# Kernel optimization log

Hardware: AMD Instinct MI355X
Metric: run time of the kernel (lower is better)

The kernel has to match this reference:

```python
import jax, jax.numpy as jnp
import numpy as np

NEG_SLOPE = 0.2  # PyG GATConv default negative_slope


def gat_conv(x, src, dst, num_nodes, W, att_src, att_dst, bias, heads, out_ch, concat):
    """PyG-style GATConv (eval mode, self-loops already included in src/dst).
    x: [N, in]; W: [in, heads*out_ch]; att_*: [heads, out_ch]; bias: [heads*out_ch] or [out_ch].
    """
    N = num_nodes
    h = (x @ W).reshape(N, heads, out_ch)                      # [N, H, C]
    a_src = jnp.sum(h * att_src[None], axis=-1)                 # [N, H]
    a_dst = jnp.sum(h * att_dst[None], axis=-1)                 # [N, H]
    e = a_src[src] + a_dst[dst]                                 # [E, H]
    e = jnp.where(e > 0, e, NEG_SLOPE * e)                      # leaky_relu
    # segment softmax over incoming edges of each destination node
    m = jax.ops.segment_max(e, dst, num_segments=N)             # [N, H]
    w = jnp.exp(e - m[dst])                                     # [E, H]
    denom = jax.ops.segment_sum(w, dst, num_segments=N)         # [N, H]
    alpha = w / denom[dst]                                      # [E, H]
    out = jax.ops.segment_sum(h[src] * alpha[:, :, None], dst, num_segments=N)  # [N, H, C]
    if concat:
        out = out.reshape(N, heads * out_ch)
    else:
        out = out.mean(axis=1)
    return out + bias


def setup_inputs() -> dict:
    key = jax.random.key(0)
    ks = jax.random.split(key, 20)
    N, T, F_IN = 100000, 50, 10
    E = 1600000
    H1, C1 = 4, 32          # conv1: heads=4, hidden=32 -> 128
    LAT = 64                # latent_dim

    def g(k, shape, scale):
        return (jax.random.normal(k, shape, dtype=jnp.float32) * scale)

    inp = {
        "temporal_data": jax.random.normal(ks[0], (N, T, F_IN), dtype=jnp.float32),
        "x": jax.random.normal(ks[1], (N, F_IN), dtype=jnp.float32),
        "edge_index": jax.random.randint(ks[2], (2, E), 0, N, dtype=jnp.int32),
        # temporal encoder: Linear(10,64) -> ReLU -> Linear(64,64)
        "tW1": g(ks[3], (F_IN, 64), 0.3), "tb1": jnp.zeros((64,), jnp.float32),
        "tW2": g(ks[4], (64, LAT), 0.12), "tb2": jnp.zeros((LAT,), jnp.float32),
        # GATConv1: in=10, out=32, heads=4, concat
        "gW1": g(ks[5], (F_IN, H1 * C1), 0.3),
        "ga1_src": g(ks[6], (H1, C1), 0.17), "ga1_dst": g(ks[7], (H1, C1), 0.17),
        "gb1": jnp.zeros((H1 * C1,), jnp.float32),
        # GATConv2: in=128, out=64, heads=1, concat=False
        "gW2": g(ks[8], (H1 * C1, LAT), 0.09),
        "ga2_src": g(ks[9], (1, LAT), 0.12), "ga2_dst": g(ks[10], (1, LAT), 0.12),
        "gb2": jnp.zeros((LAT,), jnp.float32),
        # classifier: Linear(128,64) -> ReLU -> (Dropout eval) -> Linear(64,1) -> Sigmoid
        "cW1": g(ks[11], (2 * LAT, 64), 0.09), "cb1": jnp.zeros((64,), jnp.float32),
        "cW2": g(ks[12], (64, 1), 0.12), "cb2": jnp.zeros((1,), jnp.float32),
    }
    return inp


def reference(temporal_data, x, edge_index, tW1, tb1, tW2, tb2,
              gW1, ga1_src, ga1_dst, gb1, gW2, ga2_src, ga2_dst, gb2,
              cW1, cb1, cW2, cb2):
    N = x.shape[0]
    # temporal encoder then mean over time axis (dim=1)
    t = jax.nn.relu(temporal_data @ tW1 + tb1) @ tW2 + tb2      # [N, T, 64]
    t = t.mean(axis=1)                                           # [N, 64]
    # add self-loops (PyG GATConv default add_self_loops=True)
    loop = jnp.arange(N, dtype=edge_index.dtype)
    src = jnp.concatenate([edge_index[0], loop])
    dst = jnp.concatenate([edge_index[1], loop])
    h = gat_conv(x, src, dst, N, gW1, ga1_src, ga1_dst, gb1, heads=4, out_ch=32, concat=True)
    h = jax.nn.elu(h)
    g = gat_conv(h, src, dst, N, gW2, ga2_src, ga2_dst, gb2, heads=1, out_ch=64, concat=False)  # [N, 64]
    combined = jnp.concatenate([t, g], axis=-1)                  # [N, 128]
    z = jax.nn.relu(combined @ cW1 + cb1) @ cW2 + cb2            # [N, 1]
    return jax.nn.sigmoid(z)
```

## Files before the change

kernel.cpp:

```cpp
#include <hip/hip_runtime.h>
#include <hip/hip_bf16.h>

#define DEV_INLINE __device__ __forceinline__

typedef __attribute__((ext_vector_type(8))) short short8v;
typedef __attribute__((ext_vector_type(4))) float f32x4;

DEV_INLINE float lrelu(float v) { return fmaxf(v, 0.2f * v); }

DEV_INLINE unsigned int cvt_pk_bf16(float lo, float hi) {
    unsigned int r;
    asm("v_cvt_pk_bf16_f32 %0, %1, %2" : "=v"(r) : "v"(lo), "v"(hi));
    return r;
}

DEV_INLINE unsigned short f2bf_rne(float f) {
    unsigned int b = __float_as_uint(f);
    return (unsigned short)((b + 0x7FFFu + ((b >> 16) & 1u)) >> 16);
}

DEV_INLINE unsigned int pack_bf16(float lo, float hi) {
    return (unsigned int)f2bf_rne(lo) | ((unsigned int)f2bf_rne(hi) << 16);
}

DEV_INLINE float bf_lo(unsigned int u) { return __uint_as_float(u << 16); }
DEV_INLINE float bf_hi(unsigned int u) { return __uint_as_float(u & 0xFFFF0000u); }

__global__ __launch_bounds__(1024) void k_scan1(const int* __restrict__ counts,
                                                int* __restrict__ rowptr,
                                                int* __restrict__ partials, int N) {
    __shared__ int sd[1024];
    int li = threadIdx.x;
    int i  = blockIdx.x * 1024 + li;
    int v  = (i < N) ? counts[i] : 0;
    sd[li] = v;
    __syncthreads();
    for (int off = 1; off < 1024; off <<= 1) {
        int t = (li >= off) ? sd[li - off] : 0;
        __syncthreads();
        sd[li] += t;
        __syncthreads();
    }
    int inc = sd[li];
    if (i < N) rowptr[i + 1] = inc;
    if (li == 1023) partials[blockIdx.x] = inc;
}

__global__ void k_scan3(int* __restrict__ rowptr, const int* __restrict__ partials,
                        int* __restrict__ nxt, int N) {
    int i = blockIdx.x * blockDim.x + threadIdx.x;
    if (i > N) return;
    int v;
    if (i == 0) { v = 0; rowptr[0] = 0; }
    else {
        int blk = (i - 1) >> 10;
        int pp = 0;
        for (int b = 0; b < blk; ++b) pp += partials[b];
        v = rowptr[i] + pp;
        rowptr[i] = v;
    }
    if (i < N) nxt[i] = v;
}

#define SC_K 8
#define SC_P 16
__global__ __launch_bounds__(256) void k_scatter(const int* __restrict__ ei,
                                                 int* __restrict__ nxt,
                                                 int* __restrict__ col,
                                                 int E, int range) {
    int t = threadIdx.x;
    int base = blockIdx.x * (256 * SC_K);
    int s[SC_K], d[SC_K];
#pragma unroll
    for (int k = 0; k < SC_K; ++k) {
        int e = base + k * 256 + t;
        bool v = (e < E);
        s[k] = v ? ei[e] : 0;
        d[k] = v ? ei[E + e] : -1;
    }
    int lo = 0;
    for (int p = 0; p < SC_P; ++p, lo += range) {
        int hi = lo + range;
#pragma unroll
        for (int k = 0; k < SC_K; ++k) {
            if (d[k] >= lo && d[k] < hi) {
                int pos = atomicAdd(&nxt[d[k]], 1);
                col[pos] = s[k];
            }
        }
        __syncthreads();
    }
}

__global__ __launch_bounds__(256) void k_temporal(const float* __restrict__ td,
                                                  const float* __restrict__ tW1,
                                                  const float* __restrict__ tb1,
                                                  const int* __restrict__ ei,
                                                  int* __restrict__ counts,
                                                  const float* __restrict__ tW2,
                                                  const float* __restrict__ cW1,
                                                  const float* __restrict__ tb2,
                                                  const float* __restrict__ cb1,
                                                  unsigned short* __restrict__ Wf,
                                                  float* __restrict__ bcf,
                                                  unsigned short* __restrict__ mb,
                                                  int N, int E) {
    __shared__ float lds[4][2][512];
    int tid = threadIdx.x, lane = tid & 63, wv = tid >> 6;
    int gid = blockIdx.x * 256 + tid;

    int estr = gridDim.x * 256;
    for (int e = gid; e < E; e += estr) atomicAdd(&counts[ei[E + e]], 1);

    if (gid < 4096) {
        int i = gid >> 6, c = gid & 63;
        float s = 0.f;
#pragma unroll 8
        for (int k = 0; k < 64; ++k) s = fmaf(tW2[i * 64 + k], cW1[k * 64 + c], s);
        Wf[gid] = f2bf_rne(s);
    } else if (gid < 8192) {
        Wf[gid] = f2bf_rne(cW1[gid]);
    } else if (gid < 8256) {
        int c = gid - 8192;
        float s = cb1[c];
#pragma unroll 8
        for (int k = 0; k < 64; ++k) s = fmaf(tb2[k], cW1[k * 64 + c], s);
        bcf[c] = s;
    }

    int wid  = blockIdx.x * 4 + wv;
    int nwav = gridDim.x * 4;
    int col  = lane & 15;
    int g    = lane >> 4;

    int chunk = (N + nwav - 1) / nwav;
    int n0 = wid * chunk;
    int n1 = min(n0 + chunk, N);
    if (n0 >= n1) return;
    int cnt = n1 - n0;

    short8v B[4];
#pragma unroll
    for (int cb = 0; cb < 4; ++cb) {
        union { short8v v; unsigned short u[8]; } bu;
#pragma unroll
        for (int j = 0; j < 8; ++j) {
            int f = g * 8 + j;
            int c = cb * 16 + col;
            float w = (f < 10) ? tW1[f * 64 + c] : ((f == 10) ? tb1[c] : 0.f);
            bu.u[j] = f2bf_rne(w);
        }
        B[cb] = bu.v;
    }

    float* buf0 = lds[wv][0];
    float* buf1 = lds[wv][1];

    {
        const float4* r4 = reinterpret_cast<const float4*>(td + (size_t)n0 * 500);
        float4 va = r4[lane];
        float4 vb = (lane < 61) ? r4[64 + lane] : make_float4(0.f, 0.f, 0.f, 0.f);
        *reinterpret_cast<float4*>(buf0 + 4 * lane) = va;
        if (lane < 61) *reinterpret_cast<float4*>(buf0 + 256 + 4 * lane) = vb;
    }
    float4 va = make_float4(0.f, 0.f, 0.f, 0.f), vb = va;
    if (cnt > 1) {
        const float4* rn = reinterpret_cast<const float4*>(td + (size_t)(n0 + 1) * 500);
        va = rn[lane];
        if (lane < 61) vb = rn[64 + lane];
    }

    for (int i = 0; i < cnt; ++i) {
        int n = n0 + i;
        float* wb  = (i & 1) ? buf1 : buf0;
        float* wbn = (i & 1) ? buf0 : buf1;

        if (i + 1 < cnt) {
            *reinterpret_cast<float4*>(wbn + 4 * lane) = va;
            if (lane < 61) *reinterpret_cast<float4*>(wbn + 256 + 4 * lane) = vb;
        }
        if (i + 2 < cnt) {
            const float4* rn = reinterpret_cast<const float4*>(td + (size_t)(n + 2) * 500);
            va = rn[lane];
            if (lane < 61) vb = rn[64 + lane];
        }

        float sum0 = 0.f, sum1 = 0.f, sum2 = 0.f, sum3 = 0.f;
#pragma unroll
        for (int tt = 0; tt < 4; ++tt) {
            int t = tt * 16 + col;
            bool valid = (t < 50);
            float x0 = 0.f, x1 = 0.f, x2 = 0.f, x3 = 0.f;
            float x4 = 0.f, x5 = 0.f, x6 = 0.f, x7 = 0.f;
            const float* rp = wb + t * 10;
            if (g == 0 && valid) {
                float2 p0 = *reinterpret_cast<const float2*>(rp);
                float2 p1 = *reinterpret_cast<const float2*>(rp + 2);
                float2 p2 = *reinterpret_cast<const float2*>(rp + 4);
                float2 p3 = *reinterpret_cast<const float2*>(rp + 6);
                x0 = p0.x; x1 = p0.y; x2 = p1.x; x3 = p1.y;
                x4 = p2.x; x5 = p2.y; x6 = p3.x; x7 = p3.y;
            } else if (g == 1 && valid) {
                float2 p4 = *reinterpret_cast<const float2*>(rp + 8);
                x0 = p4.x; x1 = p4.y; x2 = 1.0f;
            }
            union { short8v v; unsigned int w[4]; } au;
            au.w[0] = cvt_pk_bf16(x0, x1);
            au.w[1] = cvt_pk_bf16(x2, x3);
            au.w[2] = cvt_pk_bf16(x4, x5);
            au.w[3] = cvt_pk_bf16(x6, x7);

            f32x4 z = {0.f, 0.f, 0.f, 0.f};
            f32x4 c0 = __builtin_amdgcn_mfma_f32_16x16x32_bf16(au.v, B[0], z, 0, 0, 0);
            f32x4 c1 = __builtin_amdgcn_mfma_f32_16x16x32_bf16(au.v, B[1], z, 0, 0, 0);
            f32x4 c2 = __builtin_amdgcn_mfma_f32_16x16x32_bf16(au.v, B[2], z, 0, 0, 0);
            f32x4 c3 = __builtin_amdgcn_mfma_f32_16x16x32_bf16(au.v, B[3], z, 0, 0, 0);
#pragma unroll
            for (int i2 = 0; i2 < 4; ++i2) {
                sum0 += fmaxf(c0[i2], 0.f);
                sum1 += fmaxf(c1[i2], 0.f);
                sum2 += fmaxf(c2[i2], 0.f);
                sum3 += fmaxf(c3[i2], 0.f);
            }
        }
        sum0 += __shfl_xor(sum0, 16); sum0 += __shfl_xor(sum0, 32);
        sum1 += __shfl_xor(sum1, 16); sum1 += __shfl_xor(sum1, 32);
        sum2 += __shfl_xor(sum2, 16); sum2 += __shfl_xor(sum2, 32);
        sum3 += __shfl_xor(sum3, 16); sum3 += __shfl_xor(sum3, 32);
        float mv = (g == 0) ? sum0 : (g == 1) ? sum1 : (g == 2) ? sum2 : sum3;
        mb[(size_t)n * 64 + lane] = f2bf_rne(mv * 0.02f);
    }
}

__global__ __launch_bounds__(256) void k_g1a(const float* __restrict__ x,
                                             const float* __restrict__ gW1,
                                             const float* __restrict__ as_w,
                                             const float* __restrict__ ad_w,
                                             unsigned short* __restrict__ h1b,
                                             float* __restrict__ a1s,
                                             float* __restrict__ a1d, int N) {
    int tid = threadIdx.x, lane = tid & 63;
    int n0 = blockIdx.x * 4 + (tid >> 6);
    int n  = __builtin_amdgcn_readfirstlane(n0 < N ? n0 : N - 1);

    float wa[10], wb[10];
#pragma unroll
    for (int i = 0; i < 10; ++i) { wa[i] = gW1[i * 128 + lane]; wb[i] = gW1[i * 128 + 64 + lane]; }
    const float* xp = x + (size_t)n * 10;
    float ha = 0.f, hb = 0.f;
#pragma unroll
    for (int i = 0; i < 10; ++i) { float xv = xp[i]; ha = fmaf(xv, wa[i], ha); hb = fmaf(xv, wb[i], hb); }

    int c = lane & 31;
    int headA = lane >> 5;
    float ps_a = ha * as_w[headA * 32 + c];
    float ps_b = hb * as_w[(headA + 2) * 32 + c];
    float pd_a = ha * ad_w[headA * 32 + c];
    float pd_b = hb * ad_w[(headA + 2) * 32 + c];
#pragma unroll
    for (int m = 1; m < 32; m <<= 1) {
        ps_a += __shfl_xor(ps_a, m); ps_b += __shfl_xor(ps_b, m);
        pd_a += __shfl_xor(pd_a, m); pd_b += __shfl_xor(pd_b, m);
    }
    if (n0 < N) {
        h1b[(size_t)n * 128 + lane]      = f2bf_rne(ha);
        h1b[(size_t)n * 128 + 64 + lane] = f2bf_rne(hb);
        if (c == 0) {
            a1s[n * 4 + headA]     = ps_a;
            a1s[n * 4 + 2 + headA] = ps_b;
            a1d[n * 4 + headA]     = pd_a;
            a1d[n * 4 + 2 + headA] = pd_b;
        }
    }
}

__global__ __launch_bounds__(256) void k_g1b(const int* __restrict__ rowptr,
                                             const int* __restrict__ col,
                                             const unsigned int* __restrict__ h1u,
                                             const float* __restrict__ a1s,
                                             const float* __restrict__ a1d,
                                             const float* __restrict__ gb1,
                                             unsigned int* __restrict__ out1u, int N) {
    int tid = threadIdx.x, lane = tid & 63;
    int n0 = blockIdx.x * 4 + (tid >> 6);
    int n  = __builtin_amdgcn_readfirstlane(n0 < N ? n0 : N - 1);

    int start = rowptr[n], end = rowptr[n + 1];
    int q = lane >> 4, c = lane & 15;
    int hsel = c >> 2;
    float advh = a1d[n * 4 + hsel];
    const uint4* h1q = reinterpret_cast<const uint4*>(h1u);

    float den = 0.f;
    float a0 = 0.f, a1v = 0.f, a2v = 0.f, a3v = 0.f;
    float a4 = 0.f, a5 = 0.f, a6 = 0.f, a7 = 0.f;
    if (q == 0) {
        float w = __expf(lrelu(a1s[n * 4 + hsel] + advh));
        uint4 u = h1q[(size_t)n * 16 + c];
        den = w;
        a0 = w * bf_lo(u.x); a1v = w * bf_hi(u.x);
        a2v = w * bf_lo(u.y); a3v = w * bf_hi(u.y);
        a4 = w * bf_lo(u.z); a5 = w * bf_hi(u.z);
        a6 = w * bf_lo(u.w); a7 = w * bf_hi(u.w);
    }
    int e = start + q;
    for (; e + 4 < end; e += 8) {
        int s0 = col[e], s1 = col[e + 4];
        float q0 = a1s[s0 * 4 + hsel];
        float q1 = a1s[s1 * 4 + hsel];
        uint4 u0 = h1q[(size_t)s0 * 16 + c];
        uint4 u1 = h1q[(size_t)s1 * 16 + c];
        float w0 = __expf(lrelu(q0 + advh));
        float w1 = __expf(lrelu(q1 + advh));
        den += w0 + w1;
        a0 = fmaf(w0, bf_lo(u0.x), a0); a1v = fmaf(w0, bf_hi(u0.x), a1v);
        a2v = fmaf(w0, bf_lo(u0.y), a2v); a3v = fmaf(w0, bf_hi(u0.y), a3v);
        a4 = fmaf(w0, bf_lo(u0.z), a4); a5 = fmaf(w0, bf_hi(u0.z), a5);
        a6 = fmaf(w0, bf_lo(u0.w), a6); a7 = fmaf(w0, bf_hi(u0.w), a7);
        a0 = fmaf(w1, bf_lo(u1.x), a0); a1v = fmaf(w1, bf_hi(u1.x), a1v);
        a2v = fmaf(w1, bf_lo(u1.y), a2v); a3v = fmaf(w1, bf_hi(u1.y), a3v);
        a4 = fmaf(w1, bf_lo(u1.z), a4); a5 = fmaf(w1, bf_hi(u1.z), a5);
        a6 = fmaf(w1, bf_lo(u1.w), a6); a7 = fmaf(w1, bf_hi(u1.w), a7);
    }
    if (e < end) {
        int s = col[e];
        float qv = a1s[s * 4 + hsel];
        uint4 u = h1q[(size_t)s * 16 + c];
        float w = __expf(lrelu(qv + advh));
        den += w;
        a0 = fmaf(w, bf_lo(u.x), a0); a1v = fmaf(w, bf_hi(u.x), a1v);
        a2v = fmaf(w, bf_lo(u.y), a2v); a3v = fmaf(w, bf_hi(u.y), a3v);
        a4 = fmaf(w, bf_lo(u.z), a4); a5 = fmaf(w, bf_hi(u.z), a5);
        a6 = fmaf(w, bf_lo(u.w), a6); a7 = fmaf(w, bf_hi(u.w), a7);
    }
#define RED2(v) v += __shfl_xor(v, 16); v += __shfl_xor(v, 32);
    RED2(den) RED2(a0) RED2(a1v) RED2(a2v) RED2(a3v)
    RED2(a4) RED2(a5) RED2(a6) RED2(a7)
#undef RED2

    if (n0 < N && lane < 16) {
        float inv = 1.f / den;
        float v0 = a0 * inv + gb1[8 * c + 0];
        float v1 = a1v * inv + gb1[8 * c + 1];
        float v2 = a2v * inv + gb1[8 * c + 2];
        float v3 = a3v * inv + gb1[8 * c + 3];
        float v4 = a4 * inv + gb1[8 * c + 4];
        float v5 = a5 * inv + gb1[8 * c + 5];
        float v6 = a6 * inv + gb1[8 * c + 6];
        float v7 = a7 * inv + gb1[8 * c + 7];
        v0 = (v0 > 0.f) ? v0 : (__expf(v0) - 1.f);
        v1 = (v1 > 0.f) ? v1 : (__expf(v1) - 1.f);
        v2 = (v2 > 0.f) ? v2 : (__expf(v2) - 1.f);
        v3 = (v3 > 0.f) ? v3 : (__expf(v3) - 1.f);
        v4 = (v4 > 0.f) ? v4 : (__expf(v4) - 1.f);
        v5 = (v5 > 0.f) ? v5 : (__expf(v5) - 1.f);
        v6 = (v6 > 0.f) ? v6 : (__expf(v6) - 1.f);
        v7 = (v7 > 0.f) ? v7 : (__expf(v7) - 1.f);
        uint4 o;
        o.x = pack_bf16(v0, v1); o.y = pack_bf16(v2, v3);
        o.z = pack_bf16(v4, v5); o.w = pack_bf16(v6, v7);
        *reinterpret_cast<uint4*>(out1u + (size_t)n * 64 + 4 * c) = o;
    }
}

__global__ __launch_bounds__(256) void k_g2a(const unsigned short* __restrict__ out1b,
                                             const float* __restrict__ gW2,
                                             const float* __restrict__ a2sw,
                                             const float* __restrict__ a2dw,
                                             unsigned short* __restrict__ h2b,
                                             float* __restrict__ a2s,
                                             float* __restrict__ a2d, int N) {
    int lane = threadIdx.x & 63;
    int wid  = (blockIdx.x * blockDim.x + threadIdx.x) >> 6;
    int nwav = (gridDim.x * blockDim.x) >> 6;
    int col = lane & 15, g4 = lane >> 4;

    short8v Bf[4][4];
#pragma unroll
    for (int ks = 0; ks < 4; ++ks)
#pragma unroll
        for (int cb = 0; cb < 4; ++cb) {
            union { short8v v; unsigned short u[8]; } bu;
#pragma unroll
            for (int j = 0; j < 8; ++j)
                bu.u[j] = f2bf_rne(gW2[(ks * 32 + g4 * 8 + j) * 64 + cb * 16 + col]);
            Bf[ks][cb] = bu.v;
        }
    float asv[4], adv[4];
#pragma unroll
    for (int cb = 0; cb < 4; ++cb) { asv[cb] = a2sw[cb * 16 + col]; adv[cb] = a2dw[cb * 16 + col]; }

    int ntile = (N + 15) >> 4;
    for (int t = wid; t < ntile; t += nwav) {
        int n0 = t * 16;
        int node = n0 + col; if (node >= N) node = N - 1;
        const unsigned short* xr = out1b + (size_t)node * 128;
        f32x4 acc0 = {0.f, 0.f, 0.f, 0.f}, acc1 = acc0, acc2 = acc0, acc3 = acc0;
#pragma unroll
        for (int ks = 0; ks < 4; ++ks) {
            short8v a = *reinterpret_cast<const short8v*>(xr + ks * 32 + g4 * 8);
            acc0 = __builtin_amdgcn_mfma_f32_16x16x32_bf16(a, Bf[ks][0], acc0, 0, 0, 0);
            acc1 = __builtin_amdgcn_mfma_f32_16x16x32_bf16(a, Bf[ks][1], acc1, 0, 0, 0);
            acc2 = __builtin_amdgcn_mfma_f32_16x16x32_bf16(a, Bf[ks][2], acc2, 0, 0, 0);
            acc3 = __builtin_amdgcn_mfma_f32_16x16x32_bf16(a, Bf[ks][3], acc3, 0, 0, 0);
        }
        float ps[4] = {0.f, 0.f, 0.f, 0.f}, pd[4] = {0.f, 0.f, 0.f, 0.f};
#define G2A_EPI(CB, ACC)                                                      \
        {                                                                     \
            _Pragma("unroll")                                                 \
            for (int i = 0; i < 4; ++i) {                                     \
                float v = ACC[i];                                             \
                int r = n0 + g4 * 4 + i;                                      \
                if (r < N) h2b[(size_t)r * 64 + CB * 16 + col] = f2bf_rne(v); \
                ps[i] = fmaf(v, asv[CB], ps[i]);                              \
                pd[i] = fmaf(v, adv[CB], pd[i]);                              \
            }                                                                 \
        }
        G2A_EPI(0, acc0) G2A_EPI(1, acc1) G2A_EPI(2, acc2) G2A_EPI(3, acc3)
#undef G2A_EPI
#pragma unroll
        for (int i = 0; i < 4; ++i) {
            ps[i] += __shfl_xor(ps[i], 1); ps[i] += __shfl_xor(ps[i], 2);
            ps[i] += __shfl_xor(ps[i], 4); ps[i] += __shfl_xor(ps[i], 8);
            pd[i] += __shfl_xor(pd[i], 1); pd[i] += __shfl_xor(pd[i], 2);
            pd[i] += __shfl_xor(pd[i], 4); pd[i] += __shfl_xor(pd[i], 8);
        }
        if (col == 0) {
#pragma unroll
            for (int i = 0; i < 4; ++i) {
                int r = n0 + g4 * 4 + i;
                if (r < N) { a2s[r] = ps[i]; a2d[r] = pd[i]; }
            }
        }
    }
}

__global__ __launch_bounds__(256) void k_g2b(const int* __restrict__ rowptr,
                                             const int* __restrict__ col,
                                             const unsigned int* __restrict__ h2u,
                                             const float* __restrict__ a2s,
                                             const float* __restrict__ a2d,
                                             const float* __restrict__ gb2,
                                             unsigned int* __restrict__ gu, int N) {
    int tid = threadIdx.x, lane = tid & 63;
    int n0 = blockIdx.x * 4 + (tid >> 6);
    int n  = __builtin_amdgcn_readfirstlane(n0 < N ? n0 : N - 1);

    int start = rowptr[n], end = rowptr[n + 1];
    int q = lane >> 3, c = lane & 7;
    float ad = a2d[n];
    const uint4* h2q = reinterpret_cast<const uint4*>(h2u);

    float den = 0.f;
    float a0 = 0.f, a1v = 0.f, a2v = 0.f, a3v = 0.f;
    float a4 = 0.f, a5 = 0.f, a6 = 0.f, a7 = 0.f;
    if (q == 0) {
        float w = __expf(lrelu(a2s[n] + ad));
        uint4 u = h2q[(size_t)n * 8 + c];
        den = w;
        a0 = w * bf_lo(u.x); a1v = w * bf_hi(u.x);
        a2v = w * bf_lo(u.y); a3v = w * bf_hi(u.y);
        a4 = w * bf_lo(u.z); a5 = w * bf_hi(u.z);
        a6 = w * bf_lo(u.w); a7 = w * bf_hi(u.w);
    }
    for (int e = start + q; e < end; e += 8) {
        int s = col[e];
        float w = __expf(lrelu(a2s[s] + ad));
        uint4 u = h2q[(size_t)s * 8 + c];
        den += w;
        a0 = fmaf(w, bf_lo(u.x), a0); a1v = fmaf(w, bf_hi(u.x), a1v);
        a2v = fmaf(w, bf_lo(u.y), a2v); a3v = fmaf(w, bf_hi(u.y), a3v);
        a4 = fmaf(w, bf_lo(u.z), a4); a5 = fmaf(w, bf_hi(u.z), a5);
        a6 = fmaf(w, bf_lo(u.w), a6); a7 = fmaf(w, bf_hi(u.w), a7);
    }
#define RED3(v) v += __shfl_xor(v, 8); v += __shfl_xor(v, 16); v += __shfl_xor(v, 32);
    RED3(den) RED3(a0) RED3(a1v) RED3(a2v) RED3(a3v)
    RED3(a4) RED3(a5) RED3(a6) RED3(a7)
#undef RED3

    if (n0 < N && lane < 8) {
        float inv = 1.f / den;
        uint4 o;
        o.x = pack_bf16(a0 * inv + gb2[8 * c + 0], a1v * inv + gb2[8 * c + 1]);
        o.y = pack_bf16(a2v * inv + gb2[8 * c + 2], a3v * inv + gb2[8 * c + 3]);
        o.z = pack_bf16(a4 * inv + gb2[8 * c + 4], a5 * inv + gb2[8 * c + 5]);
        o.w = pack_bf16(a6 * inv + gb2[8 * c + 6], a7 * inv + gb2[8 * c + 7]);
        *reinterpret_cast<uint4*>(gu + (size_t)n * 32 + 4 * c) = o;
    }
}

__global__ __launch_bounds__(256) void k_cls(const unsigned short* __restrict__ mb,
                                             const unsigned short* __restrict__ gb,
                                             const unsigned short* __restrict__ Wf,
                                             const float* __restrict__ bc,
                                             const float* __restrict__ cW2,
                                             const float* __restrict__ cb2,
                                             float* __restrict__ out, int N) {
    int lane = threadIdx.x & 63;
    int wid  = (blockIdx.x * blockDim.x + threadIdx.x) >> 6;
    int nwav = (gridDim.x * blockDim.x) >> 6;
    int col = lane & 15, g4 = lane >> 4;

    short8v Bf[4][4];
#pragma unroll
    for (int ks = 0; ks < 4; ++ks)
#pragma unroll
        for (int cb = 0; cb < 4; ++cb) {
            union { short8v v; unsigned short u[8]; } bu;
#pragma unroll
            for (int j = 0; j < 8; ++j)
                bu.u[j] = Wf[(ks * 32 + g4 * 8 + j) * 64 + cb * 16 + col];
            Bf[ks][cb] = bu.v;
        }
    float w2v[4], bcv[4];
#pragma unroll
    for (int cb = 0; cb < 4; ++cb) { w2v[cb] = cW2[cb * 16 + col]; bcv[cb] = bc[cb * 16 + col]; }
    float cb2v = cb2[0];

    int ntile = (N + 15) >> 4;
    for (int t = wid; t < ntile; t += nwav) {
        int n0 = t * 16;
        int node = n0 + col; if (node >= N) node = N - 1;
        const unsigned short* mr = mb + (size_t)node * 64;
        const unsigned short* gr = gb + (size_t)node * 64;
        f32x4 acc0 = {0.f, 0.f, 0.f, 0.f}, acc1 = acc0, acc2 = acc0, acc3 = acc0;
#pragma unroll
        for (int ks = 0; ks < 4; ++ks) {
            short8v a = (ks < 2)
                ? *reinterpret_cast<const short8v*>(mr + ks * 32 + g4 * 8)
                : *reinterpret_cast<const short8v*>(gr + (ks - 2) * 32 + g4 * 8);
            acc0 = __builtin_amdgcn_mfma_f32_16x16x32_bf16(a, Bf[ks][0], acc0, 0, 0, 0);
            acc1 = __builtin_amdgcn_mfma_f32_16x16x32_bf16(a, Bf[ks][1], acc1, 0, 0, 0);
            acc2 = __builtin_amdgcn_mfma_f32_16x16x32_bf16(a, Bf[ks][2], acc2, 0, 0, 0);
            acc3 = __builtin_amdgcn_mfma_f32_16x16x32_bf16(a, Bf[ks][3], acc3, 0, 0, 0);
        }
        float z[4] = {0.f, 0.f, 0.f, 0.f};
#define CLS_EPI(CB, ACC)                                                   \
        {                                                                  \
            _Pragma("unroll")                                              \
            for (int i = 0; i < 4; ++i)                                    \
                z[i] = fmaf(fmaxf(ACC[i] + bcv[CB], 0.f), w2v[CB], z[i]);  \
        }
        CLS_EPI(0, acc0) CLS_EPI(1, acc1) CLS_EPI(2, acc2) CLS_EPI(3, acc3)
#undef CLS_EPI
#pragma unroll
        for (int i = 0; i < 4; ++i) {
            z[i] += __shfl_xor(z[i], 1); z[i] += __shfl_xor(z[i], 2);
            z[i] += __shfl_xor(z[i], 4); z[i] += __shfl_xor(z[i], 8);
        }
        if (col == 0) {
#pragma unroll
            for (int i = 0; i < 4; ++i) {
                int r = n0 + g4 * 4 + i;
                if (r < N) out[r] = 1.f / (1.f + __expf(-(z[i] + cb2v)));
            }
        }
    }
}

extern "C" void kernel_launch(void* const* d_in, const int* in_sizes, int n_in,
                              void* d_out, int out_size, void* d_ws, size_t ws_size,
                              hipStream_t stream) {
    const float* td   = (const float*)d_in[0];
    const float* x    = (const float*)d_in[1];
    const int*   ei   = (const int*)d_in[2];
    const float* tW1  = (const float*)d_in[3];
    const float* tb1  = (const float*)d_in[4];
    const float* tW2  = (const float*)d_in[5];
    const float* tb2  = (const float*)d_in[6];
    const float* gW1  = (const float*)d_in[7];
    const float* ga1s = (const float*)d_in[8];
    const float* ga1d = (const float*)d_in[9];
    const float* gb1  = (const float*)d_in[10];
    const float* gW2  = (const float*)d_in[11];
    const float* ga2s = (const float*)d_in[12];
    const float* ga2d = (const float*)d_in[13];
    const float* gb2  = (const float*)d_in[14];
    const float* cW1  = (const float*)d_in[15];
    const float* cb1  = (const float*)d_in[16];
    const float* cW2  = (const float*)d_in[17];
    const float* cb2  = (const float*)d_in[18];

    int N = in_sizes[1] / 10;
    int E = in_sizes[2] / 2;

    float* fws = (float*)d_ws;
    unsigned short* mb16   = (unsigned short*)fws;
    unsigned short* h1b    = (unsigned short*)(fws + (size_t)N * 32);
    unsigned short* out1b  = (unsigned short*)(fws + (size_t)N * 96);
    float* a1s   = fws + (size_t)N * 160;
    float* a1d   = fws + (size_t)N * 164;
    unsigned short* h2b = h1b;
    float* a2s   = a1s;
    float* a2d   = a1d;
    unsigned short* gb16 = out1b;

    int* ib       = (int*)(fws + (size_t)N * 168);
    int* counts   = ib;
    int* rowptr   = ib + N;
    int* nxt      = ib + 2 * N + 1;
    int* partials = ib + 3 * N + 1;
    int* col      = ib + 3 * N + 1 + 128;

    unsigned short* Wf = (unsigned short*)(col + E);
    float* bcf = (float*)(Wf + 8192);

    hipMemsetAsync(counts, 0, (size_t)N * sizeof(int), stream);

    int NB = (N + 1023) / 1024;
    int range = (N + SC_P - 1) / SC_P;
    int nb4   = (N + 3) / 4;
    int ntile = (N + 15) / 16;
    int nbt   = (ntile + 3) / 4;

    k_temporal<<<2048, 256, 0, stream>>>(td, tW1, tb1, ei, counts,
                                         tW2, cW1, tb2, cb1, Wf, bcf, mb16, N, E);
    k_scan1  <<<NB, 1024, 0, stream>>>(counts, rowptr, partials, N);
    k_scan3  <<<(N + 1 + 255) / 256, 256, 0, stream>>>(rowptr, partials, nxt, N);
    k_scatter<<<(E + 256 * SC_K - 1) / (256 * SC_K), 256, 0, stream>>>(ei, nxt, col, E, range);

    k_g1a<<<nb4, 256, 0, stream>>>(x, gW1, ga1s, ga1d, h1b, a1s, a1d, N);
    k_g1b<<<nb4, 256, 0, stream>>>(rowptr, col, (const unsigned int*)h1b, a1s, a1d, gb1,
                                   (unsigned int*)out1b, N);
    k_g2a<<<nbt, 256, 0, stream>>>(out1b, gW2, ga2s, ga2d, h2b, a2s, a2d, N);
    k_g2b<<<nb4, 256, 0, stream>>>(rowptr, col, (const unsigned int*)h2b, a2s, a2d, gb2,
                                   (unsigned int*)gb16, N);
    k_cls<<<nbt, 256, 0, stream>>>(mb16, gb16, Wf, bcf, cW2, cb2, (float*)d_out, N);
}
```

Before: 399.2 us.

## Read temporal rows directly from global memory instead of LDS double buffering

The temporal encoder kernel no longer stages each node's 500-float row into per-wave LDS double buffers with register prefetch. Each wave now loops over nodes in a grid-stride pattern and loads its inputs straight from global memory with float2 reads. This removes the LDS traffic, the bookkeeping and the contiguous chunk partitioning, but gives up the explicit prefetch overlap and the coalesced float4 loads, so it relies on caches to absorb the strided small reads.

```diff
diff --git a/kernel.cpp b/kernel.cpp
--- a/kernel.cpp
+++ b/kernel.cpp
@@ -105,8 +105,7 @@
                                                   float* __restrict__ bcf,
                                                   unsigned short* __restrict__ mb,
                                                   int N, int E) {
-    __shared__ float lds[4][2][512];
-    int tid = threadIdx.x, lane = tid & 63, wv = tid >> 6;
+    int tid = threadIdx.x, lane = tid & 63;
     int gid = blockIdx.x * 256 + tid;
 
     int estr = gridDim.x * 256;
@@ -128,16 +127,10 @@
         bcf[c] = s;
     }
 
-    int wid  = blockIdx.x * 4 + wv;
-    int nwav = gridDim.x * 4;
+    int wid  = gid >> 6;
+    int nwav = (gridDim.x * 256) >> 6;
     int col  = lane & 15;
     int g    = lane >> 4;
-
-    int chunk = (N + nwav - 1) / nwav;
-    int n0 = wid * chunk;
-    int n1 = min(n0 + chunk, N);
-    if (n0 >= n1) return;
-    int cnt = n1 - n0;
 
     short8v B[4];
 #pragma unroll
@@ -153,38 +146,8 @@
         B[cb] = bu.v;
     }
 
-    float* buf0 = lds[wv][0];
-    float* buf1 = lds[wv][1];
-
-    {
-        const float4* r4 = reinterpret_cast<const float4*>(td + (size_t)n0 * 500);
-        float4 va = r4[lane];
-        float4 vb = (lane < 61) ? r4[64 + lane] : make_float4(0.f, 0.f, 0.f, 0.f);
-        *reinterpret_cast<float4*>(buf0 + 4 * lane) = va;
-        if (lane < 61) *reinterpret_cast<float4*>(buf0 + 256 + 4 * lane) = vb;
-    }
-    float4 va = make_float4(0.f, 0.f, 0.f, 0.f), vb = va;
-    if (cnt > 1) {
-        const float4* rn = reinterpret_cast<const float4*>(td + (size_t)(n0 + 1) * 500);
-        va = rn[lane];
-        if (lane < 61) vb = rn[64 + lane];
-    }
-
-    for (int i = 0; i < cnt; ++i) {
-        int n = n0 + i;
-        float* wb  = (i & 1) ? buf1 : buf0;
-        float* wbn = (i & 1) ? buf0 : buf1;
-
-        if (i + 1 < cnt) {
-            *reinterpret_cast<float4*>(wbn + 4 * lane) = va;
-            if (lane < 61) *reinterpret_cast<float4*>(wbn + 256 + 4 * lane) = vb;
-        }
-        if (i + 2 < cnt) {
-            const float4* rn = reinterpret_cast<const float4*>(td + (size_t)(n + 2) * 500);
-            va = rn[lane];
-            if (lane < 61) vb = rn[64 + lane];
-        }
-
+    for (int n = wid; n < N; n += nwav) {
+        const float* base = td + (size_t)n * 500;
         float sum0 = 0.f, sum1 = 0.f, sum2 = 0.f, sum3 = 0.f;
 #pragma unroll
         for (int tt = 0; tt < 4; ++tt) {
@@ -192,7 +155,7 @@
             bool valid = (t < 50);
             float x0 = 0.f, x1 = 0.f, x2 = 0.f, x3 = 0.f;
             float x4 = 0.f, x5 = 0.f, x6 = 0.f, x7 = 0.f;
-            const float* rp = wb + t * 10;
+            const float* rp = base + t * 10;
             if (g == 0 && valid) {
                 float2 p0 = *reinterpret_cast<const float2*>(rp);
                 float2 p1 = *reinterpret_cast<const float2*>(rp + 2);
@@ -216,11 +179,11 @@
             f32x4 c2 = __builtin_amdgcn_mfma_f32_16x16x32_bf16(au.v, B[2], z, 0, 0, 0);
             f32x4 c3 = __builtin_amdgcn_mfma_f32_16x16x32_bf16(au.v, B[3], z, 0, 0, 0);
 #pragma unroll
-            for (int i2 = 0; i2 < 4; ++i2) {
-                sum0 += fmaxf(c0[i2], 0.f);
-                sum1 += fmaxf(c1[i2], 0.f);
-                sum2 += fmaxf(c2[i2], 0.f);
-                sum3 += fmaxf(c3[i2], 0.f);
+            for (int i = 0; i < 4; ++i) {
+                sum0 += fmaxf(c0[i], 0.f);
+                sum1 += fmaxf(c1[i], 0.f);
+                sum2 += fmaxf(c2[i], 0.f);
+                sum3 += fmaxf(c3[i], 0.f);
             }
         }
         sum0 += __shfl_xor(sum0, 16); sum0 += __shfl_xor(sum0, 32);
```

After: 420.1 us. 5.3% more time.
